# Performance work log

Hardware: AMD Instinct MI355X
Metric: run time of the kernel (lower is better)

The kernel has to match this reference:

```python
import jax, jax.numpy as jnp
import numpy as np

TOP_K = 2
NUM_EXPERTS = 8
EPS = 1e-9


def setup_inputs() -> dict:
    key = jax.random.key(0)
    ks = jax.random.split(key, 6)
    B, S, H, E, F = 2, 1024, 1024, NUM_EXPERTS, 512
    hidden_states = jax.random.normal(ks[0], (B, S, H), dtype=jnp.float32)
    gate_w = jax.random.normal(ks[1], (E, H), dtype=jnp.float32) * 0.02
    gate_up_proj = jax.random.normal(ks[2], (E, H, 2 * F), dtype=jnp.float32) * 0.02
    down_proj = jax.random.normal(ks[3], (E, F, H), dtype=jnp.float32) * 0.02
    # modality in {-1, 0, 1}: -1 text, 1 vision, 0 special/unassigned
    token_modality = (jax.random.randint(ks[4], (B * S,), 0, 3) - 1).astype(jnp.int32)
    expert_modality = (jax.random.randint(ks[5], (E,), 0, 3) - 1).astype(jnp.int32)
    return {
        "hidden_states": hidden_states,
        "gate_w": gate_w,
        "gate_up_proj": gate_up_proj,
        "down_proj": down_proj,
        "token_modality": token_modality,
        "expert_modality": expert_modality,
    }


def reference(hidden_states, gate_w, gate_up_proj, down_proj, token_modality, expert_modality):
    B, S, H = hidden_states.shape
    bs = B * S
    E, K = NUM_EXPERTS, TOP_K
    x = hidden_states.reshape(bs, H)

    # ---- router: GEMM + softmax + top-k + renorm ----
    router_logits = x @ gate_w.T                              # [bs, E]
    probs = jax.nn.softmax(router_logits, axis=-1)
    rw, sel = jax.lax.top_k(probs, K)                         # [bs, K]
    rw = rw / jnp.sum(rw, axis=-1, keepdims=True)

    # ---- modality-masked expert skip (prefill branch: seq_length > 1) ----
    tok_mod_slots = jnp.broadcast_to(token_modality[:, None], (bs, K))  # [bs, K]
    exp_mod_slots = expert_modality[sel]                                # [bs, K]
    valid = (tok_mod_slots != 0) & (exp_mod_slots != 0)
    mismatch = valid & ((tok_mod_slots * exp_mod_slots) == -1)

    sel_flat = sel.reshape(-1)
    valid_count = jax.ops.segment_sum(valid.reshape(-1).astype(jnp.int32), sel_flat, num_segments=E)
    mismatch_count = jax.ops.segment_sum(mismatch.reshape(-1).astype(jnp.int32), sel_flat, num_segments=E)
    skip_expert = (valid_count > 0) & (mismatch_count == valid_count) & (expert_modality != 0)

    zero_mask = skip_expert[sel]                              # [bs, K]
    rw = jnp.where(zero_mask, 0.0, rw)
    sum_w2 = jnp.sum(rw, axis=-1, keepdims=True)
    rw = jnp.where(sum_w2 > 0, rw / jnp.maximum(sum_w2, EPS), rw)

    # ---- scatter top-k weights into dense [bs, E] routing matrix ----
    dense_w = jnp.zeros((bs, E), dtype=rw.dtype).at[jnp.arange(bs)[:, None], sel].set(rw)

    # ---- fused experts: SiLU-gated MLP per expert, combined by routing weights ----
    gu = jnp.einsum("th,ehf->tef", x, gate_up_proj)           # [bs, E, 2F]
    g, u = jnp.split(gu, 2, axis=-1)
    act = jax.nn.silu(g) * u                                  # [bs, E, F]
    out = jnp.einsum("tef,efh,te->th", act, down_proj, dense_w)
    return out.reshape(B, S, H)
```

## Files before the change

kernel.cpp:

```cpp
#include <hip/hip_runtime.h>
#include <math.h>

#define BS 2048
#define H  1024
#define E  8
#define F  512

typedef __attribute__((ext_vector_type(8))) short bf16x8;
typedef __attribute__((ext_vector_type(4))) float f32x4;
typedef unsigned short u16;
typedef unsigned int u32;

__device__ inline u16 f2bf(float f) {
    u32 u = __float_as_uint(f);
    return (u16)((u + 0x7fffu + ((u >> 16) & 1u)) >> 16);
}

__device__ __forceinline__ void async_cp16(const u16* g, u16* l) {
    __builtin_amdgcn_global_load_lds(
        (const __attribute__((address_space(1))) void*)g,
        (__attribute__((address_space(3))) void*)l, 16, 0, 0);
}


__global__ __launch_bounds__(256) void prep_router_kernel(
    const float* __restrict__ gup, const float* __restrict__ dwn,
    u16* __restrict__ gt, u16* __restrict__ dt,
    const float* __restrict__ x, const float* __restrict__ gate_w,
    const int* __restrict__ tok_mod, const int* __restrict__ exp_mod,
    int2* __restrict__ sel_out, float2* __restrict__ w_out,
    u16* __restrict__ xb, float* __restrict__ out)
{
    int b = blockIdx.x;
    int tid = threadIdx.x;

    if (b < 3072) {
        const float* src; u16* dst_base; int e, kt, nt, K, Nn;
        if (b < 2048) {
            e = b >> 8; int rem = b & 255; kt = rem >> 4; nt = rem & 15;
            src = gup + (size_t)e * 1048576; dst_base = gt + (size_t)e * 1048576; K = 1024; Nn = 1024;
        } else {
            int b2 = b - 2048; e = b2 >> 7; int rem = b2 & 127; kt = rem >> 4; nt = rem & 15;
            src = dwn + (size_t)e * 524288; dst_base = dt + (size_t)e * 524288; K = 512; Nn = 1024;
        }
        int k0 = kt * 64, n0 = nt * 64;
        __shared__ float t[64][68];
        int r = tid >> 2, c4 = tid & 3;
        const float* srow = src + (size_t)(k0 + r) * Nn + n0 + c4 * 16;
#pragma unroll
        for (int i = 0; i < 4; i++) {
            float4 v = *(const float4*)(srow + i * 4);
            *(float4*)&t[r][c4 * 16 + i * 4] = v;
        }
        __syncthreads();
        u16 o[16];
#pragma unroll
        for (int m = 0; m < 16; m++) o[m] = f2bf(t[c4 * 16 + m][r]);
        u16* dst = dst_base + (size_t)(n0 + r) * K + k0 + c4 * 16;
        uint4 q0, q1;
        q0.x = (u32)o[0] | ((u32)o[1] << 16);  q0.y = (u32)o[2] | ((u32)o[3] << 16);
        q0.z = (u32)o[4] | ((u32)o[5] << 16);  q0.w = (u32)o[6] | ((u32)o[7] << 16);
        q1.x = (u32)o[8] | ((u32)o[9] << 16);  q1.y = (u32)o[10] | ((u32)o[11] << 16);
        q1.z = (u32)o[12] | ((u32)o[13] << 16); q1.w = (u32)o[14] | ((u32)o[15] << 16);
        *(uint4*)dst = q0;
        *(uint4*)(dst + 8) = q1;
        return;
    }

    int wv = tid >> 6, lane = tid & 63;
    int token = (b - 3072) * 4 + wv;
    float4 z = make_float4(0.f, 0.f, 0.f, 0.f);
    float4* orow4 = (float4*)(out + (size_t)token * H);
#pragma unroll
    for (int i = 0; i < 4; i++) orow4[lane + 64 * i] = z;

    const float4* xr4 = (const float4*)(x + (size_t)token * H);
    const float4* gw4 = (const float4*)gate_w;
    float acc[E];
#pragma unroll
    for (int e = 0; e < E; e++) acc[e] = 0.f;
#pragma unroll
    for (int i = 0; i < 4; i++) {
        int idx = lane + 64 * i;
        float4 xv = xr4[idx];
        ushort4 pk;
        pk.x = f2bf(xv.x); pk.y = f2bf(xv.y); pk.z = f2bf(xv.z); pk.w = f2bf(xv.w);
        *(ushort4*)(xb + (size_t)token * H + idx * 4) = pk;
#pragma unroll
        for (int e = 0; e < E; e++) {
            float4 g = gw4[e * 256 + idx];
            acc[e] += xv.x * g.x + xv.y * g.y + xv.z * g.z + xv.w * g.w;
        }
    }
#pragma unroll
    for (int e = 0; e < E; e++) {
#pragma unroll
        for (int off = 32; off > 0; off >>= 1) acc[e] += __shfl_down(acc[e], off, 64);
    }
    if (lane == 0) {
        float m = acc[0];
#pragma unroll
        for (int e = 1; e < E; e++) m = fmaxf(m, acc[e]);
        float p[E]; float s = 0.f;
#pragma unroll
        for (int e = 0; e < E; e++) { p[e] = expf(acc[e] - m); s += p[e]; }
        float inv = 1.f / s;
#pragma unroll
        for (int e = 0; e < E; e++) p[e] *= inv;
        int i0 = 0; float p0 = p[0];
#pragma unroll
        for (int e = 1; e < E; e++) if (p[e] > p0) { p0 = p[e]; i0 = e; }
        int i1 = -1; float p1 = -1.f;
#pragma unroll
        for (int e = 0; e < E; e++) if (e != i0 && p[e] > p1) { p1 = p[e]; i1 = e; }
        float rs = 1.f / (p0 + p1);
        float w0 = p0 * rs, w1 = p1 * rs;
        int tm = tok_mod[token];
        int em0 = exp_mod[i0], em1 = exp_mod[i1];
        int v0 = (tm != 0) && (em0 != 0);
        int v1 = (tm != 0) && (em1 != 0);
        int mm0 = v0 && (tm * em0 == -1);
        int mm1 = v1 && (tm * em1 == -1);
        sel_out[token] = make_int2(i0 | (v0 << 8) | (mm0 << 9),
                                   i1 | (v1 << 8) | (mm1 << 9));
        w_out[token] = make_float2(w0, w1);
    }
}

__global__ __launch_bounds__(1024) void finalize_kernel(
    const int* __restrict__ exp_mod, int* __restrict__ counters,
    const int2* __restrict__ sel_in, const float2* __restrict__ w_in,
    int* __restrict__ tok_list, float* __restrict__ w_list)
{
    __shared__ int vcnt[E], mcnt[E], gpos[E];
    int tid = threadIdx.x;
    if (tid < E) { vcnt[tid] = 0; mcnt[tid] = 0; gpos[tid] = 0; }
    __syncthreads();
#pragma unroll
    for (int h = 0; h < 2; h++) {
        int t = tid + h * 1024;
        int2 s = sel_in[t];
        int i0 = s.x & 7, i1 = s.y & 7;
        if (s.x & 256) atomicAdd(&vcnt[i0], 1);
        if (s.x & 512) atomicAdd(&mcnt[i0], 1);
        if (s.y & 256) atomicAdd(&vcnt[i1], 1);
        if (s.y & 512) atomicAdd(&mcnt[i1], 1);
    }
    __syncthreads();
    bool skip[E];
#pragma unroll
    for (int e = 0; e < E; e++)
        skip[e] = (vcnt[e] > 0) && (mcnt[e] == vcnt[e]) && (exp_mod[e] != 0);
#pragma unroll
    for (int h = 0; h < 2; h++) {
        int t = tid + h * 1024;
        int2 s = sel_in[t];
        int i0 = s.x & 7, i1 = s.y & 7;
        float2 w = w_in[t];
        float w0 = skip[i0] ? 0.f : w.x;
        float w1 = skip[i1] ? 0.f : w.y;
        float sm = w0 + w1;
        if (sm > 0.f) { float inv = 1.f / fmaxf(sm, 1e-9f); w0 *= inv; w1 *= inv; }
        if (w0 > 0.f) {
            int pos = atomicAdd(&gpos[i0], 1);
            tok_list[i0 * BS + pos] = t; w_list[i0 * BS + pos] = w0;
        }
        if (w1 > 0.f) {
            int pos = atomicAdd(&gpos[i1], 1);
            tok_list[i1 * BS + pos] = t; w_list[i1 * BS + pos] = w1;
        }
    }
    __syncthreads();
    if (tid < E) counters[16 + tid] = gpos[tid];
}

__global__ __launch_bounds__(256) void gu_mfma_kernel(
    const u16* __restrict__ xb, const u16* __restrict__ gup_t,
    const int* __restrict__ counters, const int* __restrict__ tok_list,
    const float* __restrict__ w_list, u16* __restrict__ act)
{
    int e = blockIdx.z;
    int n = counters[16 + e];
    int t0 = blockIdx.y * 64;
    if (t0 >= n) return;
    int f0 = blockIdx.x * 64;
    int base = 0;
#pragma unroll
    for (int i = 0; i < E; i++) if (i < e) base += counters[16 + i];

    __shared__ __align__(16) u16 Asl[2][64 * 64];
    __shared__ __align__(16) u16 Bsl[2][128 * 64];

    int tid = threadIdx.x;
    int wv = tid >> 6, lane = tid & 63;
    int l16 = lane & 15, quad = lane >> 4;
    int wm = wv & 1, wn = wv >> 1;

    int lr = lane >> 3, lc = lane & 7;
    int r0 = wv * 8 + lr, r1 = r0 + 32;
    int tokA0 = tok_list[e * BS + min(t0 + r0, n - 1)];
    int tokA1 = tok_list[e * BS + min(t0 + r1, n - 1)];
    const u16* agp0 = xb + (size_t)tokA0 * H + (size_t)((lc ^ (r0 & 7)) * 8);
    const u16* agp1 = xb + (size_t)tokA1 * H + (size_t)((lc ^ (r1 & 7)) * 8);
    int alo0 = r0 * 64 + lc * 8, alo1 = r1 * 64 + lc * 8;
    const u16* gb = gup_t + ((size_t)e << 20);
    const u16* bgp[4]; int blo[4];
#pragma unroll
    for (int j = 0; j < 4; j++) {
        int c = j * 32 + wv * 8 + lr;
        int gcol = (c < 64) ? (f0 + c) : (512 + f0 + (c - 64));
        bgp[j] = gb + (size_t)gcol * H + (size_t)((lc ^ (c & 7)) * 8);
        blo[j] = c * 64 + lc * 8;
    }

    f32x4 acc[2][4];
#pragma unroll
    for (int i = 0; i < 2; i++)
#pragma unroll
        for (int j = 0; j < 4; j++) acc[i][j] = (f32x4){0.f, 0.f, 0.f, 0.f};

    async_cp16(agp0, &Asl[0][alo0]);
    async_cp16(agp1, &Asl[0][alo1]);
#pragma unroll
    for (int j = 0; j < 4; j++) async_cp16(bgp[j], &Bsl[0][blo[j]]);

    int sw = l16 & 7;
    int p = 0;
    for (int k0 = 0; k0 < H; k0 += 64) {
        __syncthreads();
        if (k0 + 64 < H) {
            int q = p ^ 1;
            async_cp16(agp0 + k0 + 64, &Asl[q][alo0]);
            async_cp16(agp1 + k0 + 64, &Asl[q][alo1]);
#pragma unroll
            for (int j = 0; j < 4; j++) async_cp16(bgp[j] + k0 + 64, &Bsl[q][blo[j]]);
        }
#pragma unroll
        for (int s = 0; s < 2; s++) {
            int ch = ((s * 4 + quad) ^ sw) * 8;
            bf16x8 af[2], bfr[4];
#pragma unroll
            for (int i = 0; i < 2; i++)
                af[i] = *(const bf16x8*)&Asl[p][(wm * 32 + i * 16 + l16) * 64 + ch];
#pragma unroll
            for (int j = 0; j < 4; j++) {
                int col = (j < 2) ? (wn * 32 + j * 16 + l16) : (64 + wn * 32 + (j - 2) * 16 + l16);
                bfr[j] = *(const bf16x8*)&Bsl[p][col * 64 + ch];
            }
#pragma unroll
            for (int i = 0; i < 2; i++)
#pragma unroll
                for (int j = 0; j < 4; j++)
                    acc[i][j] = __builtin_amdgcn_mfma_f32_16x16x32_bf16(af[i], bfr[j], acc[i][j], 0, 0, 0);
        }
        p ^= 1;
    }
#pragma unroll
    for (int i = 0; i < 2; i++)
#pragma unroll
        for (int r = 0; r < 4; r++) {
            int R = t0 + wm * 32 + i * 16 + quad * 4 + r;
            if (R < n) {
                float w = w_list[e * BS + R];
                size_t rowoff = (size_t)(base + R) * F + f0 + wn * 32 + l16;
#pragma unroll
                for (int j = 0; j < 2; j++) {
                    float g = acc[i][j][r], u = acc[i][j + 2][r];
                    float v = (g / (1.f + expf(-g))) * u * w;
                    act[rowoff + j * 16] = f2bf(v);
                }
            }
        }
}

__global__ __launch_bounds__(256) void down_mfma_kernel(
    const u16* __restrict__ act, const u16* __restrict__ down_t,
    const int* __restrict__ counters, const int* __restrict__ tok_list,
    float* __restrict__ out)
{
    int e = blockIdx.z;
    int n = counters[16 + e];
    int t0 = blockIdx.y * 64;
    if (t0 >= n) return;
    int h0 = blockIdx.x * 128;
    int base = 0;
#pragma unroll
    for (int i = 0; i < E; i++) if (i < e) base += counters[16 + i];

    __shared__ __align__(16) u16 Asl[2][64 * 64];
    __shared__ __align__(16) u16 Bsl[2][128 * 64];

    int tid = threadIdx.x;
    int wv = tid >> 6, lane = tid & 63;
    int l16 = lane & 15, quad = lane >> 4;
    int wm = wv & 1, wn = wv >> 1;

    int lr = lane >> 3, lc = lane & 7;
    int r0 = wv * 8 + lr, r1 = r0 + 32;
    const u16* agp0 = act + (size_t)(base + min(t0 + r0, n - 1)) * F + (size_t)((lc ^ (r0 & 7)) * 8);
    const u16* agp1 = act + (size_t)(base + min(t0 + r1, n - 1)) * F + (size_t)((lc ^ (r1 & 7)) * 8);
    int alo0 = r0 * 64 + lc * 8, alo1 = r1 * 64 + lc * 8;
    const u16* db = down_t + ((size_t)e << 19);
    const u16* bgp[4]; int blo[4];
#pragma unroll
    for (int j = 0; j < 4; j++) {
        int c = j * 32 + wv * 8 + lr;
        bgp[j] = db + (size_t)(h0 + c) * F + (size_t)((lc ^ (c & 7)) * 8);
        blo[j] = c * 64 + lc * 8;
    }

    f32x4 acc[2][4];
#pragma unroll
    for (int i = 0; i < 2; i++)
#pragma unroll
        for (int j = 0; j < 4; j++) acc[i][j] = (f32x4){0.f, 0.f, 0.f, 0.f};

    async_cp16(agp0, &Asl[0][alo0]);
    async_cp16(agp1, &Asl[0][alo1]);
#pragma unroll
    for (int j = 0; j < 4; j++) async_cp16(bgp[j], &Bsl[0][blo[j]]);

    int sw = l16 & 7;
    int p = 0;
    for (int k0 = 0; k0 < F; k0 += 64) {
        __syncthreads();
        if (k0 + 64 < F) {
            int q = p ^ 1;
            async_cp16(agp0 + k0 + 64, &Asl[q][alo0]);
            async_cp16(agp1 + k0 + 64, &Asl[q][alo1]);
#pragma unroll
            for (int j = 0; j < 4; j++) async_cp16(bgp[j] + k0 + 64, &Bsl[q][blo[j]]);
        }
#pragma unroll
        for (int s = 0; s < 2; s++) {
            int ch = ((s * 4 + quad) ^ sw) * 8;
            bf16x8 af[2], bfr[4];
#pragma unroll
            for (int i = 0; i < 2; i++)
                af[i] = *(const bf16x8*)&Asl[p][(wm * 32 + i * 16 + l16) * 64 + ch];
#pragma unroll
            for (int j = 0; j < 4; j++)
                bfr[j] = *(const bf16x8*)&Bsl[p][(wn * 64 + j * 16 + l16) * 64 + ch];
#pragma unroll
            for (int i = 0; i < 2; i++)
#pragma unroll
                for (int j = 0; j < 4; j++)
                    acc[i][j] = __builtin_amdgcn_mfma_f32_16x16x32_bf16(af[i], bfr[j], acc[i][j], 0, 0, 0);
        }
        p ^= 1;
    }
#pragma unroll
    for (int i = 0; i < 2; i++)
#pragma unroll
        for (int r = 0; r < 4; r++) {
            int R = t0 + wm * 32 + i * 16 + quad * 4 + r;
            if (R < n) {
                int tok = tok_list[e * BS + R];
                float* orow = out + (size_t)tok * H + h0 + wn * 64 + l16;
#pragma unroll
                for (int j = 0; j < 4; j++)
                    atomicAdd(&orow[j * 16], acc[i][j][r]);
            }
        }
}

extern "C" void kernel_launch(void* const* d_in, const int* in_sizes, int n_in,
                              void* d_out, int out_size, void* d_ws, size_t ws_size,
                              hipStream_t stream)
{
    const float* x       = (const float*)d_in[0];
    const float* gate_w  = (const float*)d_in[1];
    const float* gup     = (const float*)d_in[2];
    const float* down    = (const float*)d_in[3];
    const int*   tok_mod = (const int*)d_in[4];
    const int*   exp_mod = (const int*)d_in[5];
    float* out = (float*)d_out;

    char* ws = (char*)d_ws;
    int*    counters = (int*)ws;
    int2*   sel      = (int2*)(ws + 4096);
    float2* wsel     = (float2*)(ws + 20480);
    int*    tok_list = (int*)(ws + 36864);
    float*  w_list   = (float*)(ws + 102400);
    u16*    x_bf     = (u16*)(ws + 167936);
    u16*    gup_t    = (u16*)(ws + 4362240);
    u16*    down_t   = (u16*)(ws + 21139456);
    u16*    act      = (u16*)(ws + 29528064);

    prep_router_kernel<<<3584, 256, 0, stream>>>(gup, down, gup_t, down_t,
                                                 x, gate_w, tok_mod, exp_mod,
                                                 sel, wsel, x_bf, out);
    finalize_kernel<<<1, 1024, 0, stream>>>(exp_mod, counters, sel, wsel, tok_list, w_list);
    gu_mfma_kernel<<<dim3(8, 32, E), 256, 0, stream>>>(x_bf, gup_t, counters, tok_list, w_list, act);
    down_mfma_kernel<<<dim3(8, 32, E), 256, 0, stream>>>(act, down_t, counters, tok_list, out);
}
```

Baseline: 157.3 us.

## Halve MoE GEMM token tiles and move down-proj conversion into gate-up kernel

Both expert GEMM kernels now use 32-token tiles instead of 64, with each wave owning a 16-column slice. This doubles the grid, so more blocks are available to fill the GPU when per-expert token counts are uneven. The down_proj fp32-to-bf16 transpose moves out of the prep/router kernel into extra blocks of the gate-up kernel, shortening the prep phase and overlapping that conversion with gate-up work. The cost is less B-tile reuse per block, so more weight traffic per token, and more early-exit blocks.

```diff
diff --git a/kernel.cpp b/kernel.cpp
--- a/kernel.cpp
+++ b/kernel.cpp
@@ -24,8 +24,7 @@
 
 
 __global__ __launch_bounds__(256) void prep_router_kernel(
-    const float* __restrict__ gup, const float* __restrict__ dwn,
-    u16* __restrict__ gt, u16* __restrict__ dt,
+    const float* __restrict__ gup, u16* __restrict__ gt,
     const float* __restrict__ x, const float* __restrict__ gate_w,
     const int* __restrict__ tok_mod, const int* __restrict__ exp_mod,
     int2* __restrict__ sel_out, float2* __restrict__ w_out,
@@ -34,19 +33,14 @@
     int b = blockIdx.x;
     int tid = threadIdx.x;
 
-    if (b < 3072) {
-        const float* src; u16* dst_base; int e, kt, nt, K, Nn;
-        if (b < 2048) {
-            e = b >> 8; int rem = b & 255; kt = rem >> 4; nt = rem & 15;
-            src = gup + (size_t)e * 1048576; dst_base = gt + (size_t)e * 1048576; K = 1024; Nn = 1024;
-        } else {
-            int b2 = b - 2048; e = b2 >> 7; int rem = b2 & 127; kt = rem >> 4; nt = rem & 15;
-            src = dwn + (size_t)e * 524288; dst_base = dt + (size_t)e * 524288; K = 512; Nn = 1024;
-        }
+    if (b < 2048) {
+        int e = b >> 8; int rem = b & 255; int kt = rem >> 4, nt = rem & 15;
+        const float* src = gup + (size_t)e * 1048576;
+        u16* dst_base = gt + (size_t)e * 1048576;
         int k0 = kt * 64, n0 = nt * 64;
         __shared__ float t[64][68];
         int r = tid >> 2, c4 = tid & 3;
-        const float* srow = src + (size_t)(k0 + r) * Nn + n0 + c4 * 16;
+        const float* srow = src + (size_t)(k0 + r) * 1024 + n0 + c4 * 16;
 #pragma unroll
         for (int i = 0; i < 4; i++) {
             float4 v = *(const float4*)(srow + i * 4);
@@ -56,7 +50,7 @@
         u16 o[16];
 #pragma unroll
         for (int m = 0; m < 16; m++) o[m] = f2bf(t[c4 * 16 + m][r]);
-        u16* dst = dst_base + (size_t)(n0 + r) * K + k0 + c4 * 16;
+        u16* dst = dst_base + (size_t)(n0 + r) * 1024 + k0 + c4 * 16;
         uint4 q0, q1;
         q0.x = (u32)o[0] | ((u32)o[1] << 16);  q0.y = (u32)o[2] | ((u32)o[3] << 16);
         q0.z = (u32)o[4] | ((u32)o[5] << 16);  q0.w = (u32)o[6] | ((u32)o[7] << 16);
@@ -68,7 +62,7 @@
     }
 
     int wv = tid >> 6, lane = tid & 63;
-    int token = (b - 3072) * 4 + wv;
+    int token = (b - 2048) * 4 + wv;
     float4 z = make_float4(0.f, 0.f, 0.f, 0.f);
     float4* orow4 = (float4*)(out + (size_t)token * H);
 #pragma unroll
@@ -177,32 +171,64 @@
 __global__ __launch_bounds__(256) void gu_mfma_kernel(
     const u16* __restrict__ xb, const u16* __restrict__ gup_t,
     const int* __restrict__ counters, const int* __restrict__ tok_list,
-    const float* __restrict__ w_list, u16* __restrict__ act)
+    const float* __restrict__ w_list, u16* __restrict__ act,
+    const float* __restrict__ dwn, u16* __restrict__ dt)
 {
+    __shared__ __align__(16) char smem[40960];
+    int tid = threadIdx.x;
+
+    if (blockIdx.y >= 64) {
+        float (*t)[68] = (float(*)[68])smem;
+        int hb = blockIdx.x + 8 * (blockIdx.y - 64) + 32 * blockIdx.z;
+        int r = tid >> 2, c4 = tid & 3;
+#pragma unroll
+        for (int i = 0; i < 4; i++) {
+            int tile = hb * 4 + i;
+            int e = tile >> 7; int rem = tile & 127;
+            int k0 = (rem >> 4) * 64, n0 = (rem & 15) * 64;
+            const float* srow = dwn + (size_t)e * 524288 + (size_t)(k0 + r) * 1024 + n0 + c4 * 16;
+#pragma unroll
+            for (int q = 0; q < 4; q++) {
+                float4 v = *(const float4*)(srow + q * 4);
+                *(float4*)&t[r][c4 * 16 + q * 4] = v;
+            }
+            __syncthreads();
+            u16 o[16];
+#pragma unroll
+            for (int m = 0; m < 16; m++) o[m] = f2bf(t[c4 * 16 + m][r]);
+            u16* dst = dt + (size_t)e * 524288 + (size_t)(n0 + r) * 512 + k0 + c4 * 16;
+            uint4 q0, q1;
+            q0.x = (u32)o[0] | ((u32)o[1] << 16);  q0.y = (u32)o[2] | ((u32)o[3] << 16);
+            q0.z = (u32)o[4] | ((u32)o[5] << 16);  q0.w = (u32)o[6] | ((u32)o[7] << 16);
+            q1.x = (u32)o[8] | ((u32)o[9] << 16);  q1.y = (u32)o[10] | ((u32)o[11] << 16);
+            q1.z = (u32)o[12] | ((u32)o[13] << 16); q1.w = (u32)o[14] | ((u32)o[15] << 16);
+            *(uint4*)dst = q0;
+            *(uint4*)(dst + 8) = q1;
+            __syncthreads();
+        }
+        return;
+    }
+
     int e = blockIdx.z;
     int n = counters[16 + e];
-    int t0 = blockIdx.y * 64;
+    int t0 = blockIdx.y * 32;
     if (t0 >= n) return;
     int f0 = blockIdx.x * 64;
     int base = 0;
 #pragma unroll
     for (int i = 0; i < E; i++) if (i < e) base += counters[16 + i];
 
-    __shared__ __align__(16) u16 Asl[2][64 * 64];
-    __shared__ __align__(16) u16 Bsl[2][128 * 64];
-
-    int tid = threadIdx.x;
+    u16 (*Asl)[32 * 64] = (u16(*)[32 * 64])smem;
+    u16 (*Bsl)[128 * 64] = (u16(*)[128 * 64])(smem + 8192);
+
     int wv = tid >> 6, lane = tid & 63;
     int l16 = lane & 15, quad = lane >> 4;
-    int wm = wv & 1, wn = wv >> 1;
 
     int lr = lane >> 3, lc = lane & 7;
-    int r0 = wv * 8 + lr, r1 = r0 + 32;
-    int tokA0 = tok_list[e * BS + min(t0 + r0, n - 1)];
-    int tokA1 = tok_list[e * BS + min(t0 + r1, n - 1)];
-    const u16* agp0 = xb + (size_t)tokA0 * H + (size_t)((lc ^ (r0 & 7)) * 8);
-    const u16* agp1 = xb + (size_t)tokA1 * H + (size_t)((lc ^ (r1 & 7)) * 8);
-    int alo0 = r0 * 64 + lc * 8, alo1 = r1 * 64 + lc * 8;
+    int r0 = wv * 8 + lr;
+    int tokA = tok_list[e * BS + min(t0 + r0, n - 1)];
+    const u16* agp = xb + (size_t)tokA * H + (size_t)((lc ^ (r0 & 7)) * 8);
+    int alo = r0 * 64 + lc * 8;
     const u16* gb = gup_t + ((size_t)e << 20);
     const u16* bgp[4]; int blo[4];
 #pragma unroll
@@ -213,14 +239,13 @@
         blo[j] = c * 64 + lc * 8;
     }
 
-    f32x4 acc[2][4];
+    f32x4 acc[2][2];
 #pragma unroll
     for (int i = 0; i < 2; i++)
 #pragma unroll
-        for (int j = 0; j < 4; j++) acc[i][j] = (f32x4){0.f, 0.f, 0.f, 0.f};
-
-    async_cp16(agp0, &Asl[0][alo0]);
-    async_cp16(agp1, &Asl[0][alo1]);
+        for (int j = 0; j < 2; j++) acc[i][j] = (f32x4){0.f, 0.f, 0.f, 0.f};
+
+    async_cp16(agp, &Asl[0][alo]);
 #pragma unroll
     for (int j = 0; j < 4; j++) async_cp16(bgp[j], &Bsl[0][blo[j]]);
 
@@ -230,28 +255,24 @@
         __syncthreads();
         if (k0 + 64 < H) {
             int q = p ^ 1;
-            async_cp16(agp0 + k0 + 64, &Asl[q][alo0]);
-            async_cp16(agp1 + k0 + 64, &Asl[q][alo1]);
+            async_cp16(agp + k0 + 64, &Asl[q][alo]);
 #pragma unroll
             for (int j = 0; j < 4; j++) async_cp16(bgp[j] + k0 + 64, &Bsl[q][blo[j]]);
         }
 #pragma unroll
         for (int s = 0; s < 2; s++) {
             int ch = ((s * 4 + quad) ^ sw) * 8;
-            bf16x8 af[2], bfr[4];
+            bf16x8 af[2];
 #pragma unroll
             for (int i = 0; i < 2; i++)
-                af[i] = *(const bf16x8*)&Asl[p][(wm * 32 + i * 16 + l16) * 64 + ch];
-#pragma unroll
-            for (int j = 0; j < 4; j++) {
-                int col = (j < 2) ? (wn * 32 + j * 16 + l16) : (64 + wn * 32 + (j - 2) * 16 + l16);
-                bfr[j] = *(const bf16x8*)&Bsl[p][col * 64 + ch];
+                af[i] = *(const bf16x8*)&Asl[p][(i * 16 + l16) * 64 + ch];
+            bf16x8 bg = *(const bf16x8*)&Bsl[p][(wv * 16 + l16) * 64 + ch];
+            bf16x8 bu = *(const bf16x8*)&Bsl[p][(64 + wv * 16 + l16) * 64 + ch];
+#pragma unroll
+            for (int i = 0; i < 2; i++) {
+                acc[i][0] = __builtin_amdgcn_mfma_f32_16x16x32_bf16(af[i], bg, acc[i][0], 0, 0, 0);
+                acc[i][1] = __builtin_amdgcn_mfma_f32_16x16x32_bf16(af[i], bu, acc[i][1], 0, 0, 0);
             }
-#pragma unroll
-            for (int i = 0; i < 2; i++)
-#pragma unroll
-                for (int j = 0; j < 4; j++)
-                    acc[i][j] = __builtin_amdgcn_mfma_f32_16x16x32_bf16(af[i], bfr[j], acc[i][j], 0, 0, 0);
         }
         p ^= 1;
     }
@@ -259,16 +280,12 @@
     for (int i = 0; i < 2; i++)
 #pragma unroll
         for (int r = 0; r < 4; r++) {
-            int R = t0 + wm * 32 + i * 16 + quad * 4 + r;
+            int R = t0 + i * 16 + quad * 4 + r;
             if (R < n) {
                 float w = w_list[e * BS + R];
-                size_t rowoff = (size_t)(base + R) * F + f0 + wn * 32 + l16;
-#pragma unroll
-                for (int j = 0; j < 2; j++) {
-                    float g = acc[i][j][r], u = acc[i][j + 2][r];
-                    float v = (g / (1.f + expf(-g))) * u * w;
-                    act[rowoff + j * 16] = f2bf(v);
-                }
+                float g = acc[i][0][r], u = acc[i][1][r];
+                float v = (g / (1.f + expf(-g))) * u * w;
+                act[(size_t)(base + R) * F + f0 + wv * 16 + l16] = f2bf(v);
             }
         }
 }
@@ -280,26 +297,24 @@
 {
     int e = blockIdx.z;
     int n = counters[16 + e];
-    int t0 = blockIdx.y * 64;
+    int t0 = blockIdx.y * 32;
     if (t0 >= n) return;
     int h0 = blockIdx.x * 128;
     int base = 0;
 #pragma unroll
     for (int i = 0; i < E; i++) if (i < e) base += counters[16 + i];
 
-    __shared__ __align__(16) u16 Asl[2][64 * 64];
+    __shared__ __align__(16) u16 Asl[2][32 * 64];
     __shared__ __align__(16) u16 Bsl[2][128 * 64];
 
     int tid = threadIdx.x;
     int wv = tid >> 6, lane = tid & 63;
     int l16 = lane & 15, quad = lane >> 4;
-    int wm = wv & 1, wn = wv >> 1;
 
     int lr = lane >> 3, lc = lane & 7;
-    int r0 = wv * 8 + lr, r1 = r0 + 32;
-    const u16* agp0 = act + (size_t)(base + min(t0 + r0, n - 1)) * F + (size_t)((lc ^ (r0 & 7)) * 8);
-    const u16* agp1 = act + (size_t)(base + min(t0 + r1, n - 1)) * F + (size_t)((lc ^ (r1 & 7)) * 8);
-    int alo0 = r0 * 64 + lc * 8, alo1 = r1 * 64 + lc * 8;
+    int r0 = wv * 8 + lr;
+    const u16* agp = act + (size_t)(base + min(t0 + r0, n - 1)) * F + (size_t)((lc ^ (r0 & 7)) * 8);
+    int alo = r0 * 64 + lc * 8;
     const u16* db = down_t + ((size_t)e << 19);
     const u16* bgp[4]; int blo[4];
 #pragma unroll
@@ -309,14 +324,13 @@
         blo[j] = c * 64 + lc * 8;
     }
 
-    f32x4 acc[2][4];
+    f32x4 acc[2][2];
 #pragma unroll
     for (int i = 0; i < 2; i++)
 #pragma unroll
-        for (int j = 0; j < 4; j++) acc[i][j] = (f32x4){0.f, 0.f, 0.f, 0.f};
-
-    async_cp16(agp0, &Asl[0][alo0]);
-    async_cp16(agp1, &Asl[0][alo1]);
+        for (int j = 0; j < 2; j++) acc[i][j] = (f32x4){0.f, 0.f, 0.f, 0.f};
+
+    async_cp16(agp, &Asl[0][alo]);
 #pragma unroll
     for (int j = 0; j < 4; j++) async_cp16(bgp[j], &Bsl[0][blo[j]]);
 
@@ -326,26 +340,24 @@
         __syncthreads();
         if (k0 + 64 < F) {
             int q = p ^ 1;
-            async_cp16(agp0 + k0 + 64, &Asl[q][alo0]);
-            async_cp16(agp1 + k0 + 64, &Asl[q][alo1]);
+            async_cp16(agp + k0 + 64, &Asl[q][alo]);
 #pragma unroll
             for (int j = 0; j < 4; j++) async_cp16(bgp[j] + k0 + 64, &Bsl[q][blo[j]]);
         }
 #pragma unroll
         for (int s = 0; s < 2; s++) {
             int ch = ((s * 4 + quad) ^ sw) * 8;
-            bf16x8 af[2], bfr[4];
+            bf16x8 af[2], b0, b1;
 #pragma unroll
             for (int i = 0; i < 2; i++)
-                af[i] = *(const bf16x8*)&Asl[p][(wm * 32 + i * 16 + l16) * 64 + ch];
-#pragma unroll
-            for (int j = 0; j < 4; j++)
-                bfr[j] = *(const bf16x8*)&Bsl[p][(wn * 64 + j * 16 + l16) * 64 + ch];
-#pragma unroll
-            for (int i = 0; i < 2; i++)
-#pragma unroll
-                for (int j = 0; j < 4; j++)
-                    acc[i][j] = __builtin_amdgcn_mfma_f32_16x16x32_bf16(af[i], bfr[j], acc[i][j], 0, 0, 0);
+                af[i] = *(const bf16x8*)&Asl[p][(i * 16 + l16) * 64 + ch];
+            b0 = *(const bf16x8*)&Bsl[p][(wv * 32 + l16) * 64 + ch];
+            b1 = *(const bf16x8*)&Bsl[p][(wv * 32 + 16 + l16) * 64 + ch];
+#pragma unroll
+            for (int i = 0; i < 2; i++) {
+                acc[i][0] = __builtin_amdgcn_mfma_f32_16x16x32_bf16(af[i], b0, acc[i][0], 0, 0, 0);
+                acc[i][1] = __builtin_amdgcn_mfma_f32_16x16x32_bf16(af[i], b1, acc[i][1], 0, 0, 0);
+            }
         }
         p ^= 1;
     }
@@ -353,13 +365,12 @@
     for (int i = 0; i < 2; i++)
 #pragma unroll
         for (int r = 0; r < 4; r++) {
-            int R = t0 + wm * 32 + i * 16 + quad * 4 + r;
+            int R = t0 + i * 16 + quad * 4 + r;
             if (R < n) {
                 int tok = tok_list[e * BS + R];
-                float* orow = out + (size_t)tok * H + h0 + wn * 64 + l16;
-#pragma unroll
-                for (int j = 0; j < 4; j++)
-                    atomicAdd(&orow[j * 16], acc[i][j][r]);
+                float* orow = out + (size_t)tok * H + h0 + wv * 32 + l16;
+                atomicAdd(&orow[0],  acc[i][0][r]);
+                atomicAdd(&orow[16], acc[i][1][r]);
             }
         }
 }
@@ -387,10 +398,10 @@
     u16*    down_t   = (u16*)(ws + 21139456);
     u16*    act      = (u16*)(ws + 29528064);
 
-    prep_router_kernel<<<3584, 256, 0, stream>>>(gup, down, gup_t, down_t,
-                                                 x, gate_w, tok_mod, exp_mod,
+    prep_router_kernel<<<2560, 256, 0, stream>>>(gup, gup_t, x, gate_w, tok_mod, exp_mod,
                                                  sel, wsel, x_bf, out);
     finalize_kernel<<<1, 1024, 0, stream>>>(exp_mod, counters, sel, wsel, tok_list, w_list);
-    gu_mfma_kernel<<<dim3(8, 32, E), 256, 0, stream>>>(x_bf, gup_t, counters, tok_list, w_list, act);
-    down_mfma_kernel<<<dim3(8, 32, E), 256, 0, stream>>>(act, down_t, counters, tok_list, out);
-}
+    gu_mfma_kernel<<<dim3(8, 68, E), 256, 0, stream>>>(x_bf, gup_t, counters, tok_list, w_list, act,
+                                                       down, down_t);
+    down_mfma_kernel<<<dim3(8, 64, E), 256, 0, stream>>>(act, down_t, counters, tok_list, out);
+}
```

Result: slower. 165.6 us (+5.3%).

## Pre-pack expert weights into MFMA fragment layout and drop LDS staging in GEMMs

Applied to the files above, without the earlier changes.

The prep kernel now writes the bf16 expert weights in a fragment-blocked layout, where each 16x32 MFMA B-tile is stored as 64 contiguous 16-byte chunks. The gate-up and down GEMM kernels no longer use shared memory, async LDS copies or barriers. Each wave loads its A fragment and eight B fragments directly from global memory into registers with one-step prefetch. The aim is to remove LDS traffic and block-wide syncs, at the cost of each of the four waves re-reading the same B fragments from global/L2 with no on-chip sharing.

```diff
diff --git a/kernel.cpp b/kernel.cpp
--- a/kernel.cpp
+++ b/kernel.cpp
@@ -16,16 +16,10 @@
     return (u16)((u + 0x7fffu + ((u >> 16) & 1u)) >> 16);
 }
 
-__device__ __forceinline__ void async_cp16(const u16* g, u16* l) {
-    __builtin_amdgcn_global_load_lds(
-        (const __attribute__((address_space(1))) void*)g,
-        (__attribute__((address_space(3))) void*)l, 16, 0, 0);
-}
-
 
 __global__ __launch_bounds__(256) void prep_router_kernel(
     const float* __restrict__ gup, const float* __restrict__ dwn,
-    u16* __restrict__ gt, u16* __restrict__ dt,
+    u16* __restrict__ gf, u16* __restrict__ df,
     const float* __restrict__ x, const float* __restrict__ gate_w,
     const int* __restrict__ tok_mod, const int* __restrict__ exp_mod,
     int2* __restrict__ sel_out, float2* __restrict__ w_out,
@@ -35,35 +29,43 @@
     int tid = threadIdx.x;
 
     if (b < 3072) {
-        const float* src; u16* dst_base; int e, kt, nt, K, Nn;
+        const float* src; u16* dst_base; int kt, nt, KB;
         if (b < 2048) {
-            e = b >> 8; int rem = b & 255; kt = rem >> 4; nt = rem & 15;
-            src = gup + (size_t)e * 1048576; dst_base = gt + (size_t)e * 1048576; K = 1024; Nn = 1024;
+            int e = b >> 8; int rem = b & 255; kt = rem >> 4; nt = rem & 15;
+            src = gup + (size_t)e * 1048576; dst_base = gf + (size_t)e * 1048576; KB = 32;
         } else {
-            int b2 = b - 2048; e = b2 >> 7; int rem = b2 & 127; kt = rem >> 4; nt = rem & 15;
-            src = dwn + (size_t)e * 524288; dst_base = dt + (size_t)e * 524288; K = 512; Nn = 1024;
+            int b2 = b - 2048; int e = b2 >> 7; int rem = b2 & 127; kt = rem >> 4; nt = rem & 15;
+            src = dwn + (size_t)e * 524288; dst_base = df + (size_t)e * 524288; KB = 16;
         }
         int k0 = kt * 64, n0 = nt * 64;
         __shared__ float t[64][68];
-        int r = tid >> 2, c4 = tid & 3;
-        const float* srow = src + (size_t)(k0 + r) * Nn + n0 + c4 * 16;
-#pragma unroll
-        for (int i = 0; i < 4; i++) {
-            float4 v = *(const float4*)(srow + i * 4);
-            *(float4*)&t[r][c4 * 16 + i * 4] = v;
+        {
+            int r = tid >> 2, c4 = tid & 3;
+            const float* srow = src + (size_t)(k0 + r) * 1024 + n0 + c4 * 16;
+#pragma unroll
+            for (int i = 0; i < 4; i++) {
+                float4 v = *(const float4*)(srow + i * 4);
+                *(float4*)&t[r][c4 * 16 + i * 4] = v;
+            }
         }
         __syncthreads();
-        u16 o[16];
-#pragma unroll
-        for (int m = 0; m < 16; m++) o[m] = f2bf(t[c4 * 16 + m][r]);
-        u16* dst = dst_base + (size_t)(n0 + r) * K + k0 + c4 * 16;
-        uint4 q0, q1;
-        q0.x = (u32)o[0] | ((u32)o[1] << 16);  q0.y = (u32)o[2] | ((u32)o[3] << 16);
-        q0.z = (u32)o[4] | ((u32)o[5] << 16);  q0.w = (u32)o[6] | ((u32)o[7] << 16);
-        q1.x = (u32)o[8] | ((u32)o[9] << 16);  q1.y = (u32)o[10] | ((u32)o[11] << 16);
-        q1.z = (u32)o[12] | ((u32)o[13] << 16); q1.w = (u32)o[14] | ((u32)o[15] << 16);
-        *(uint4*)dst = q0;
-        *(uint4*)(dst + 8) = q1;
+        int fi = tid >> 5, lp = tid & 31;
+        int nbi = fi >> 1, kbi = fi & 1;
+        int nb = nt * 4 + nbi, kb = kt * 2 + kbi;
+        u16* fb = dst_base + (((size_t)nb * KB + kb) << 9);
+#pragma unroll
+        for (int h = 0; h < 2; h++) {
+            int l = lp * 2 + h;
+            int nl = nbi * 16 + (l & 15);
+            int kl = kbi * 32 + (l >> 4) * 8;
+            u16 o[8];
+#pragma unroll
+            for (int j = 0; j < 8; j++) o[j] = f2bf(t[kl + j][nl]);
+            uint4 q;
+            q.x = (u32)o[0] | ((u32)o[1] << 16); q.y = (u32)o[2] | ((u32)o[3] << 16);
+            q.z = (u32)o[4] | ((u32)o[5] << 16); q.w = (u32)o[6] | ((u32)o[7] << 16);
+            *(uint4*)(fb + l * 8) = q;
+        }
         return;
     }
 
@@ -175,7 +177,7 @@
 }
 
 __global__ __launch_bounds__(256) void gu_mfma_kernel(
-    const u16* __restrict__ xb, const u16* __restrict__ gup_t,
+    const u16* __restrict__ xb, const u16* __restrict__ gup_f,
     const int* __restrict__ counters, const int* __restrict__ tok_list,
     const float* __restrict__ w_list, u16* __restrict__ act)
 {
@@ -188,93 +190,63 @@
 #pragma unroll
     for (int i = 0; i < E; i++) if (i < e) base += counters[16 + i];
 
-    __shared__ __align__(16) u16 Asl[2][64 * 64];
-    __shared__ __align__(16) u16 Bsl[2][128 * 64];
-
     int tid = threadIdx.x;
     int wv = tid >> 6, lane = tid & 63;
     int l16 = lane & 15, quad = lane >> 4;
-    int wm = wv & 1, wn = wv >> 1;
-
-    int lr = lane >> 3, lc = lane & 7;
-    int r0 = wv * 8 + lr, r1 = r0 + 32;
-    int tokA0 = tok_list[e * BS + min(t0 + r0, n - 1)];
-    int tokA1 = tok_list[e * BS + min(t0 + r1, n - 1)];
-    const u16* agp0 = xb + (size_t)tokA0 * H + (size_t)((lc ^ (r0 & 7)) * 8);
-    const u16* agp1 = xb + (size_t)tokA1 * H + (size_t)((lc ^ (r1 & 7)) * 8);
-    int alo0 = r0 * 64 + lc * 8, alo1 = r1 * 64 + lc * 8;
-    const u16* gb = gup_t + ((size_t)e << 20);
-    const u16* bgp[4]; int blo[4];
-#pragma unroll
-    for (int j = 0; j < 4; j++) {
-        int c = j * 32 + wv * 8 + lr;
-        int gcol = (c < 64) ? (f0 + c) : (512 + f0 + (c - 64));
-        bgp[j] = gb + (size_t)gcol * H + (size_t)((lc ^ (c & 7)) * 8);
-        blo[j] = c * 64 + lc * 8;
-    }
-
-    f32x4 acc[2][4];
-#pragma unroll
-    for (int i = 0; i < 2; i++)
-#pragma unroll
-        for (int j = 0; j < 4; j++) acc[i][j] = (f32x4){0.f, 0.f, 0.f, 0.f};
-
-    async_cp16(agp0, &Asl[0][alo0]);
-    async_cp16(agp1, &Asl[0][alo1]);
-#pragma unroll
-    for (int j = 0; j < 4; j++) async_cp16(bgp[j], &Bsl[0][blo[j]]);
-
-    int sw = l16 & 7;
-    int p = 0;
-    for (int k0 = 0; k0 < H; k0 += 64) {
-        __syncthreads();
-        if (k0 + 64 < H) {
-            int q = p ^ 1;
-            async_cp16(agp0 + k0 + 64, &Asl[q][alo0]);
-            async_cp16(agp1 + k0 + 64, &Asl[q][alo1]);
-#pragma unroll
-            for (int j = 0; j < 4; j++) async_cp16(bgp[j] + k0 + 64, &Bsl[q][blo[j]]);
-        }
-#pragma unroll
-        for (int s = 0; s < 2; s++) {
-            int ch = ((s * 4 + quad) ^ sw) * 8;
-            bf16x8 af[2], bfr[4];
-#pragma unroll
-            for (int i = 0; i < 2; i++)
-                af[i] = *(const bf16x8*)&Asl[p][(wm * 32 + i * 16 + l16) * 64 + ch];
+
+    int Ra = min(t0 + wv * 16 + l16, n - 1);
+    int tok = tok_list[e * BS + Ra];
+    const u16* ap = xb + (size_t)tok * H + quad * 8;
+    const u16* bp[8];
+#pragma unroll
+    for (int j = 0; j < 8; j++) {
+        int nbj = (j < 4) ? ((f0 >> 4) + j) : (32 + (f0 >> 4) + (j - 4));
+        bp[j] = gup_f + ((size_t)e << 20) + ((size_t)nbj << 14) + (size_t)lane * 8;
+    }
+
+    f32x4 acc[8];
+#pragma unroll
+    for (int j = 0; j < 8; j++) acc[j] = (f32x4){0.f, 0.f, 0.f, 0.f};
+
+    bf16x8 aC = *(const bf16x8*)ap;
+    bf16x8 bC[8];
+#pragma unroll
+    for (int j = 0; j < 8; j++) bC[j] = *(const bf16x8*)bp[j];
+
+    for (int kb = 0; kb < 31; kb++) {
+        bf16x8 aN = *(const bf16x8*)(ap + (kb + 1) * 32);
+        bf16x8 bN[8];
+#pragma unroll
+        for (int j = 0; j < 8; j++) bN[j] = *(const bf16x8*)(bp[j] + ((kb + 1) << 9));
+#pragma unroll
+        for (int j = 0; j < 8; j++)
+            acc[j] = __builtin_amdgcn_mfma_f32_16x16x32_bf16(aC, bC[j], acc[j], 0, 0, 0);
+        aC = aN;
+#pragma unroll
+        for (int j = 0; j < 8; j++) bC[j] = bN[j];
+    }
+#pragma unroll
+    for (int j = 0; j < 8; j++)
+        acc[j] = __builtin_amdgcn_mfma_f32_16x16x32_bf16(aC, bC[j], acc[j], 0, 0, 0);
+
+#pragma unroll
+    for (int r = 0; r < 4; r++) {
+        int R = t0 + wv * 16 + quad * 4 + r;
+        if (R < n) {
+            float w = w_list[e * BS + R];
+            size_t rowoff = (size_t)(base + R) * F + f0 + l16;
 #pragma unroll
             for (int j = 0; j < 4; j++) {
-                int col = (j < 2) ? (wn * 32 + j * 16 + l16) : (64 + wn * 32 + (j - 2) * 16 + l16);
-                bfr[j] = *(const bf16x8*)&Bsl[p][col * 64 + ch];
+                float g = acc[j][r], u = acc[j + 4][r];
+                float v = (g / (1.f + expf(-g))) * u * w;
+                act[rowoff + j * 16] = f2bf(v);
             }
-#pragma unroll
-            for (int i = 0; i < 2; i++)
-#pragma unroll
-                for (int j = 0; j < 4; j++)
-                    acc[i][j] = __builtin_amdgcn_mfma_f32_16x16x32_bf16(af[i], bfr[j], acc[i][j], 0, 0, 0);
-        }
-        p ^= 1;
-    }
-#pragma unroll
-    for (int i = 0; i < 2; i++)
-#pragma unroll
-        for (int r = 0; r < 4; r++) {
-            int R = t0 + wm * 32 + i * 16 + quad * 4 + r;
-            if (R < n) {
-                float w = w_list[e * BS + R];
-                size_t rowoff = (size_t)(base + R) * F + f0 + wn * 32 + l16;
-#pragma unroll
-                for (int j = 0; j < 2; j++) {
-                    float g = acc[i][j][r], u = acc[i][j + 2][r];
-                    float v = (g / (1.f + expf(-g))) * u * w;
-                    act[rowoff + j * 16] = f2bf(v);
-                }
-            }
-        }
+        }
+    }
 }
 
 __global__ __launch_bounds__(256) void down_mfma_kernel(
-    const u16* __restrict__ act, const u16* __restrict__ down_t,
+    const u16* __restrict__ act, const u16* __restrict__ down_f,
     const int* __restrict__ counters, const int* __restrict__ tok_list,
     float* __restrict__ out)
 {
@@ -287,81 +259,55 @@
 #pragma unroll
     for (int i = 0; i < E; i++) if (i < e) base += counters[16 + i];
 
-    __shared__ __align__(16) u16 Asl[2][64 * 64];
-    __shared__ __align__(16) u16 Bsl[2][128 * 64];
-
     int tid = threadIdx.x;
     int wv = tid >> 6, lane = tid & 63;
     int l16 = lane & 15, quad = lane >> 4;
-    int wm = wv & 1, wn = wv >> 1;
-
-    int lr = lane >> 3, lc = lane & 7;
-    int r0 = wv * 8 + lr, r1 = r0 + 32;
-    const u16* agp0 = act + (size_t)(base + min(t0 + r0, n - 1)) * F + (size_t)((lc ^ (r0 & 7)) * 8);
-    const u16* agp1 = act + (size_t)(base + min(t0 + r1, n - 1)) * F + (size_t)((lc ^ (r1 & 7)) * 8);
-    int alo0 = r0 * 64 + lc * 8, alo1 = r1 * 64 + lc * 8;
-    const u16* db = down_t + ((size_t)e << 19);
-    const u16* bgp[4]; int blo[4];
-#pragma unroll
-    for (int j = 0; j < 4; j++) {
-        int c = j * 32 + wv * 8 + lr;
-        bgp[j] = db + (size_t)(h0 + c) * F + (size_t)((lc ^ (c & 7)) * 8);
-        blo[j] = c * 64 + lc * 8;
-    }
-
-    f32x4 acc[2][4];
-#pragma unroll
-    for (int i = 0; i < 2; i++)
-#pragma unroll
-        for (int j = 0; j < 4; j++) acc[i][j] = (f32x4){0.f, 0.f, 0.f, 0.f};
-
-    async_cp16(agp0, &Asl[0][alo0]);
-    async_cp16(agp1, &Asl[0][alo1]);
-#pragma unroll
-    for (int j = 0; j < 4; j++) async_cp16(bgp[j], &Bsl[0][blo[j]]);
-
-    int sw = l16 & 7;
-    int p = 0;
-    for (int k0 = 0; k0 < F; k0 += 64) {
-        __syncthreads();
-        if (k0 + 64 < F) {
-            int q = p ^ 1;
-            async_cp16(agp0 + k0 + 64, &Asl[q][alo0]);
-            async_cp16(agp1 + k0 + 64, &Asl[q][alo1]);
-#pragma unroll
-            for (int j = 0; j < 4; j++) async_cp16(bgp[j] + k0 + 64, &Bsl[q][blo[j]]);
-        }
-#pragma unroll
-        for (int s = 0; s < 2; s++) {
-            int ch = ((s * 4 + quad) ^ sw) * 8;
-            bf16x8 af[2], bfr[4];
-#pragma unroll
-            for (int i = 0; i < 2; i++)
-                af[i] = *(const bf16x8*)&Asl[p][(wm * 32 + i * 16 + l16) * 64 + ch];
-#pragma unroll
-            for (int j = 0; j < 4; j++)
-                bfr[j] = *(const bf16x8*)&Bsl[p][(wn * 64 + j * 16 + l16) * 64 + ch];
-#pragma unroll
-            for (int i = 0; i < 2; i++)
-#pragma unroll
-                for (int j = 0; j < 4; j++)
-                    acc[i][j] = __builtin_amdgcn_mfma_f32_16x16x32_bf16(af[i], bfr[j], acc[i][j], 0, 0, 0);
-        }
-        p ^= 1;
-    }
-#pragma unroll
-    for (int i = 0; i < 2; i++)
-#pragma unroll
-        for (int r = 0; r < 4; r++) {
-            int R = t0 + wm * 32 + i * 16 + quad * 4 + r;
-            if (R < n) {
-                int tok = tok_list[e * BS + R];
-                float* orow = out + (size_t)tok * H + h0 + wn * 64 + l16;
-#pragma unroll
-                for (int j = 0; j < 4; j++)
-                    atomicAdd(&orow[j * 16], acc[i][j][r]);
-            }
-        }
+
+    int Ra = min(t0 + wv * 16 + l16, n - 1);
+    const u16* ap = act + (size_t)(base + Ra) * F + quad * 8;
+    const u16* bp[8];
+#pragma unroll
+    for (int j = 0; j < 8; j++) {
+        int nbj = (h0 >> 4) + j;
+        bp[j] = down_f + ((size_t)e << 19) + ((size_t)nbj << 13) + (size_t)lane * 8;
+    }
+
+    f32x4 acc[8];
+#pragma unroll
+    for (int j = 0; j < 8; j++) acc[j] = (f32x4){0.f, 0.f, 0.f, 0.f};
+
+    bf16x8 aC = *(const bf16x8*)ap;
+    bf16x8 bC[8];
+#pragma unroll
+    for (int j = 0; j < 8; j++) bC[j] = *(const bf16x8*)bp[j];
+
+    for (int kb = 0; kb < 15; kb++) {
+        bf16x8 aN = *(const bf16x8*)(ap + (kb + 1) * 32);
+        bf16x8 bN[8];
+#pragma unroll
+        for (int j = 0; j < 8; j++) bN[j] = *(const bf16x8*)(bp[j] + ((kb + 1) << 9));
+#pragma unroll
+        for (int j = 0; j < 8; j++)
+            acc[j] = __builtin_amdgcn_mfma_f32_16x16x32_bf16(aC, bC[j], acc[j], 0, 0, 0);
+        aC = aN;
+#pragma unroll
+        for (int j = 0; j < 8; j++) bC[j] = bN[j];
+    }
+#pragma unroll
+    for (int j = 0; j < 8; j++)
+        acc[j] = __builtin_amdgcn_mfma_f32_16x16x32_bf16(aC, bC[j], acc[j], 0, 0, 0);
+
+#pragma unroll
+    for (int r = 0; r < 4; r++) {
+        int R = t0 + wv * 16 + quad * 4 + r;
+        if (R < n) {
+            int tok = tok_list[e * BS + R];
+            float* orow = out + (size_t)tok * H + h0 + l16;
+#pragma unroll
+            for (int j = 0; j < 8; j++)
+                atomicAdd(&orow[j * 16], acc[j][r]);
+        }
+    }
 }
 
 extern "C" void kernel_launch(void* const* d_in, const int* in_sizes, int n_in,
@@ -383,14 +329,14 @@
     int*    tok_list = (int*)(ws + 36864);
     float*  w_list   = (float*)(ws + 102400);
     u16*    x_bf     = (u16*)(ws + 167936);
-    u16*    gup_t    = (u16*)(ws + 4362240);
-    u16*    down_t   = (u16*)(ws + 21139456);
+    u16*    gup_f    = (u16*)(ws + 4362240);
+    u16*    down_f   = (u16*)(ws + 21139456);
     u16*    act      = (u16*)(ws + 29528064);
 
-    prep_router_kernel<<<3584, 256, 0, stream>>>(gup, down, gup_t, down_t,
+    prep_router_kernel<<<3584, 256, 0, stream>>>(gup, down, gup_f, down_f,
                                                  x, gate_w, tok_mod, exp_mod,
                                                  sel, wsel, x_bf, out);
     finalize_kernel<<<1, 1024, 0, stream>>>(exp_mod, counters, sel, wsel, tok_list, w_list);
-    gu_mfma_kernel<<<dim3(8, 32, E), 256, 0, stream>>>(x_bf, gup_t, counters, tok_list, w_list, act);
-    down_mfma_kernel<<<dim3(8, 32, E), 256, 0, stream>>>(act, down_t, counters, tok_list, out);
-}
+    gu_mfma_kernel<<<dim3(8, 32, E), 256, 0, stream>>>(x_bf, gup_f, counters, tok_list, w_list, act);
+    down_mfma_kernel<<<dim3(8, 32, E), 256, 0, stream>>>(act, down_f, counters, tok_list, out);
+}
```

Result: slower. 186.7 us (+18.7%).
